# Optimization experiments

Measured on AMD Instinct MI355X. Metric: run time of the kernel, lower is better.

Reference implementation:

```python
import jax, jax.numpy as jnp
import numpy as np

N_NODES = 50000
N_EDGES = 1600000
NODE_DIM = 64
EDGE_DIM = 32
HIDDEN = 128
OUT = 64


def setup_inputs() -> dict:
    key = jax.random.key(0)
    k1, k2, k3, k4, k5, k6, k7 = jax.random.split(key, 7)
    edge_index = jax.random.randint(k1, (2, N_EDGES), 0, N_NODES, dtype=jnp.int64 if jax.config.jax_enable_x64 else jnp.int32)
    node_features = jax.random.normal(k2, (N_NODES, NODE_DIM), dtype=jnp.float32)
    edge_features = jax.random.normal(k3, (N_EDGES, EDGE_DIM), dtype=jnp.float32)
    in_dim = EDGE_DIM + 2 * NODE_DIM
    # torch nn.Linear init scale ~ 1/sqrt(fan_in)
    W1 = jax.random.uniform(k4, (HIDDEN, in_dim), jnp.float32, -1.0, 1.0) / np.sqrt(in_dim)
    b1 = jax.random.uniform(k5, (HIDDEN,), jnp.float32, -1.0, 1.0) / np.sqrt(in_dim)
    W2 = jax.random.uniform(k6, (OUT, HIDDEN), jnp.float32, -1.0, 1.0) / np.sqrt(HIDDEN)
    b2 = jax.random.uniform(k7, (OUT,), jnp.float32, -1.0, 1.0) / np.sqrt(HIDDEN)
    return {"edge_index": edge_index, "node_features": node_features,
            "edge_features": edge_features, "W1": W1, "b1": b1, "W2": W2, "b2": b2}


def reference(edge_index, node_features, edge_features, W1, b1, W2, b2):
    src = node_features[edge_index[0]]  # [E, node_dim]
    tgt = node_features[edge_index[1]]  # [E, node_dim]
    x = jnp.concatenate([edge_features, src, tgt], axis=1)  # [E, edge_dim + 2*node_dim]
    h = jax.nn.relu(x @ W1.T + b1)  # [E, hidden]
    return h @ W2.T + b2  # [E, out]
```

## Files before the change

### kernel.cpp

```cpp
#include <hip/hip_runtime.h>

typedef __bf16 bf16x4 __attribute__((ext_vector_type(4)));
typedef __bf16 bf16x8 __attribute__((ext_vector_type(8)));
typedef float  f32x4  __attribute__((ext_vector_type(4)));

#define XS 168
#define HS 136

__device__ inline f32x4 mfma16(bf16x8 a, bf16x8 b, f32x4 c) {
  return __builtin_amdgcn_mfma_f32_16x16x32_bf16(a, b, c, 0, 0, 0);
}

struct bf2 { __bf16 h, l; };
__device__ inline bf2 split(float x) {
  bf2 r;
  r.h = (__bf16)x;
  r.l = (__bf16)(x - (float)r.h);
  return r;
}

__global__ __launch_bounds__(256, 2) void edge_mlp(
    const int* __restrict__ eidx, const float* __restrict__ nf,
    const float* __restrict__ ef, const float* __restrict__ W1,
    const float* __restrict__ b1, const float* __restrict__ W2,
    const float* __restrict__ b2, float* __restrict__ out, int E)
{
  __shared__ __bf16 sXh[64 * XS];
  __shared__ __bf16 sXl[64 * XS];
  __shared__ __bf16 sHh[64 * HS];
  __shared__ __bf16 sHl[64 * HS];

  const int tid  = threadIdx.x;
  const int lane = tid & 63;
  const int wv   = tid >> 6;
  const int l16  = lane & 15;
  const int q    = lane >> 4;

  bf16x8 w1h[2][5], w1l[2][5];
#pragma unroll
  for (int nt = 0; nt < 2; ++nt) {
    const int j = 32 * wv + 16 * nt + l16;
#pragma unroll
    for (int kc = 0; kc < 5; ++kc) {
      const float* p = W1 + j * 160 + kc * 32 + q * 8;
#pragma unroll
      for (int i = 0; i < 8; ++i) {
        bf2 s = split(p[i]);
        w1h[nt][kc][i] = s.h;
        w1l[nt][kc][i] = s.l;
      }
    }
  }
  bf16x8 w2h[4], w2l[4];
  {
    const int o = 16 * wv + l16;
#pragma unroll
    for (int kc = 0; kc < 4; ++kc) {
      const float* p = W2 + o * 128 + kc * 32 + q * 8;
#pragma unroll
      for (int i = 0; i < 8; ++i) {
        bf2 s = split(p[i]);
        w2h[kc][i] = s.h;
        w2l[kc][i] = s.l;
      }
    }
  }
  const float b1j0 = b1[32 * wv + l16];
  const float b1j1 = b1[32 * wv + 16 + l16];
  const float b2o  = b2[16 * wv + l16];

  const float4* ef4 = (const float4*)ef;
  const float4* nf4 = (const float4*)nf;

  const int eL = tid >> 2;
  const int qq = tid & 3;
  const int ntiles = (E + 63) >> 6;

  for (int tile = blockIdx.x; tile < ntiles; tile += gridDim.x) {
    const int e0 = tile << 6;

    {
      int e = e0 + eL;
      if (e >= E) e = E - 1;
      const int s = eidx[e];
      const int t = eidx[E + e];
#pragma unroll
      for (int i = 0; i < 10; ++i) {
        const int fi = qq * 10 + i;
        const float4* p = (fi < 8)  ? (ef4 + e * 8 + fi)
                        : (fi < 24) ? (nf4 + s * 16 + (fi - 8))
                                    : (nf4 + t * 16 + (fi - 24));
        const float4 v = *p;
        bf16x4 hv, lv;
        { bf2 s0 = split(v.x); hv[0] = s0.h; lv[0] = s0.l; }
        { bf2 s1 = split(v.y); hv[1] = s1.h; lv[1] = s1.l; }
        { bf2 s2 = split(v.z); hv[2] = s2.h; lv[2] = s2.l; }
        { bf2 s3 = split(v.w); hv[3] = s3.h; lv[3] = s3.l; }
        *(bf16x4*)&sXh[eL * XS + fi * 4] = hv;
        *(bf16x4*)&sXl[eL * XS + fi * 4] = lv;
      }
    }
    __syncthreads();

    f32x4 acc1[4][2];
#pragma unroll
    for (int mt = 0; mt < 4; ++mt)
#pragma unroll
      for (int nt = 0; nt < 2; ++nt)
        acc1[mt][nt] = (f32x4){0.f, 0.f, 0.f, 0.f};

#pragma unroll
    for (int kc = 0; kc < 5; ++kc) {
#pragma unroll
      for (int mt = 0; mt < 4; ++mt) {
        const bf16x8 ah = *(const bf16x8*)&sXh[(16 * mt + l16) * XS + kc * 32 + q * 8];
        const bf16x8 al = *(const bf16x8*)&sXl[(16 * mt + l16) * XS + kc * 32 + q * 8];
#pragma unroll
        for (int nt = 0; nt < 2; ++nt) {
          acc1[mt][nt] = mfma16(ah, w1h[nt][kc], acc1[mt][nt]);
          acc1[mt][nt] = mfma16(ah, w1l[nt][kc], acc1[mt][nt]);
          acc1[mt][nt] = mfma16(al, w1h[nt][kc], acc1[mt][nt]);
        }
      }
    }

#pragma unroll
    for (int mt = 0; mt < 4; ++mt) {
#pragma unroll
      for (int nt = 0; nt < 2; ++nt) {
        const int col = 32 * wv + 16 * nt + l16;
        const float bb = nt ? b1j1 : b1j0;
#pragma unroll
        for (int r = 0; r < 4; ++r) {
          float h = acc1[mt][nt][r] + bb;
          h = fmaxf(h, 0.f);
          bf2 s = split(h);
          const int row = 16 * mt + 4 * q + r;
          sHh[row * HS + col] = s.h;
          sHl[row * HS + col] = s.l;
        }
      }
    }
    __syncthreads();

    f32x4 acc2[4];
#pragma unroll
    for (int mt = 0; mt < 4; ++mt) acc2[mt] = (f32x4){0.f, 0.f, 0.f, 0.f};
#pragma unroll
    for (int kc = 0; kc < 4; ++kc) {
#pragma unroll
      for (int mt = 0; mt < 4; ++mt) {
        const bf16x8 ah = *(const bf16x8*)&sHh[(16 * mt + l16) * HS + kc * 32 + q * 8];
        const bf16x8 al = *(const bf16x8*)&sHl[(16 * mt + l16) * HS + kc * 32 + q * 8];
        acc2[mt] = mfma16(ah, w2h[kc], acc2[mt]);
        acc2[mt] = mfma16(ah, w2l[kc], acc2[mt]);
        acc2[mt] = mfma16(al, w2h[kc], acc2[mt]);
      }
    }
#pragma unroll
    for (int mt = 0; mt < 4; ++mt) {
#pragma unroll
      for (int r = 0; r < 4; ++r) {
        const int e = e0 + 16 * mt + 4 * q + r;
        if (e < E) out[e * 64 + 16 * wv + l16] = acc2[mt][r] + b2o;
      }
    }
  }
}

extern "C" void kernel_launch(void* const* d_in, const int* in_sizes, int n_in,
                              void* d_out, int out_size, void* d_ws, size_t ws_size,
                              hipStream_t stream) {
  const int*   eidx = (const int*)d_in[0];
  const float* nf   = (const float*)d_in[1];
  const float* ef   = (const float*)d_in[2];
  const float* W1   = (const float*)d_in[3];
  const float* b1   = (const float*)d_in[4];
  const float* W2   = (const float*)d_in[5];
  const float* b2   = (const float*)d_in[6];
  float* out = (float*)d_out;
  const int E = in_sizes[0] / 2;

  dim3 grid(1024), block(256);
  hipLaunchKernelGGL(edge_mlp, grid, block, 0, stream,
                     eidx, nf, ef, W1, b1, W2, b2, out, E);
}
```

Measured before the change: 896.5 us.

## Prefetch next tile's gather into registers and interleave MFMA chains

Loads the next tile's edge and node features into registers while the current tile runs its MFMAs, overlapping global gather latency with compute. The gather layout now has each thread take strided float4s instead of contiguous ones, which improves coalescing. The MFMA issue order is changed so consecutive MFMAs use independent accumulators. The hidden split is packed into one u32 per element so stores are single 32-bit writes, and it is unpacked with perm instructions before the second GEMM. The cost is ten float4 prefetch registers per thread, which may pressure occupancy under the 2-wave-per-SIMD launch bound.

```diff
diff --git a/kernel.cpp b/kernel.cpp
--- a/kernel.cpp
+++ b/kernel.cpp
@@ -3,9 +3,10 @@
 typedef __bf16 bf16x4 __attribute__((ext_vector_type(4)));
 typedef __bf16 bf16x8 __attribute__((ext_vector_type(8)));
 typedef float  f32x4  __attribute__((ext_vector_type(4)));
-
-#define XS 168
-#define HS 136
+typedef unsigned int u32x4 __attribute__((ext_vector_type(4)));
+
+#define XS  168
+#define HS2 132
 
 __device__ inline f32x4 mfma16(bf16x8 a, bf16x8 b, f32x4 c) {
   return __builtin_amdgcn_mfma_f32_16x16x32_bf16(a, b, c, 0, 0, 0);
@@ -17,6 +18,9 @@
   r.h = (__bf16)x;
   r.l = (__bf16)(x - (float)r.h);
   return r;
+}
+__device__ inline unsigned int bfbits(__bf16 x) {
+  return (unsigned int)__builtin_bit_cast(unsigned short, x);
 }
 
 __global__ __launch_bounds__(256, 2) void edge_mlp(
@@ -27,8 +31,7 @@
 {
   __shared__ __bf16 sXh[64 * XS];
   __shared__ __bf16 sXl[64 * XS];
-  __shared__ __bf16 sHh[64 * HS];
-  __shared__ __bf16 sHl[64 * HS];
+  __shared__ unsigned int sH2[64 * HS2];
 
   const int tid  = threadIdx.x;
   const int lane = tid & 63;
@@ -76,31 +79,46 @@
   const int qq = tid & 3;
   const int ntiles = (E + 63) >> 6;
 
-  for (int tile = blockIdx.x; tile < ntiles; tile += gridDim.x) {
+  float4 g[10];
+  auto gather = [&](int tile_) {
+    int e = tile_ * 64 + eL;
+    if (e >= E) e = E - 1;
+    const int s = eidx[e];
+    const int t = eidx[E + e];
+#pragma unroll
+    for (int i = 0; i < 10; ++i) {
+      const int fi = qq + 4 * i;
+      const float4* p = (i < 2) ? (ef4 + e * 8 + fi)
+                      : (i < 6) ? (nf4 + s * 16 + (fi - 8))
+                                : (nf4 + t * 16 + (fi - 24));
+      g[i] = *p;
+    }
+  };
+
+  int tile = blockIdx.x;
+  if (tile < ntiles) gather(tile);
+
+  for (; tile < ntiles; tile += gridDim.x) {
     const int e0 = tile << 6;
 
+#pragma unroll
+    for (int i = 0; i < 10; ++i) {
+      const int fi = qq + 4 * i;
+      const float4 v = g[i];
+      bf16x4 hv, lv;
+      { bf2 s0 = split(v.x); hv[0] = s0.h; lv[0] = s0.l; }
+      { bf2 s1 = split(v.y); hv[1] = s1.h; lv[1] = s1.l; }
+      { bf2 s2 = split(v.z); hv[2] = s2.h; lv[2] = s2.l; }
+      { bf2 s3 = split(v.w); hv[3] = s3.h; lv[3] = s3.l; }
+      *(bf16x4*)&sXh[eL * XS + fi * 4] = hv;
+      *(bf16x4*)&sXl[eL * XS + fi * 4] = lv;
+    }
+    __syncthreads();
+
     {
-      int e = e0 + eL;
-      if (e >= E) e = E - 1;
-      const int s = eidx[e];
-      const int t = eidx[E + e];
-#pragma unroll
-      for (int i = 0; i < 10; ++i) {
-        const int fi = qq * 10 + i;
-        const float4* p = (fi < 8)  ? (ef4 + e * 8 + fi)
-                        : (fi < 24) ? (nf4 + s * 16 + (fi - 8))
-                                    : (nf4 + t * 16 + (fi - 24));
-        const float4 v = *p;
-        bf16x4 hv, lv;
-        { bf2 s0 = split(v.x); hv[0] = s0.h; lv[0] = s0.l; }
-        { bf2 s1 = split(v.y); hv[1] = s1.h; lv[1] = s1.l; }
-        { bf2 s2 = split(v.z); hv[2] = s2.h; lv[2] = s2.l; }
-        { bf2 s3 = split(v.w); hv[3] = s3.h; lv[3] = s3.l; }
-        *(bf16x4*)&sXh[eL * XS + fi * 4] = hv;
-        *(bf16x4*)&sXl[eL * XS + fi * 4] = lv;
-      }
-    }
-    __syncthreads();
+      const int nxt = tile + gridDim.x;
+      if (nxt < ntiles) gather(nxt);
+    }
 
     f32x4 acc1[4][2];
 #pragma unroll
@@ -112,15 +130,28 @@
 #pragma unroll
     for (int kc = 0; kc < 5; ++kc) {
 #pragma unroll
-      for (int mt = 0; mt < 4; ++mt) {
-        const bf16x8 ah = *(const bf16x8*)&sXh[(16 * mt + l16) * XS + kc * 32 + q * 8];
-        const bf16x8 al = *(const bf16x8*)&sXl[(16 * mt + l16) * XS + kc * 32 + q * 8];
-#pragma unroll
-        for (int nt = 0; nt < 2; ++nt) {
-          acc1[mt][nt] = mfma16(ah, w1h[nt][kc], acc1[mt][nt]);
-          acc1[mt][nt] = mfma16(ah, w1l[nt][kc], acc1[mt][nt]);
-          acc1[mt][nt] = mfma16(al, w1h[nt][kc], acc1[mt][nt]);
+      for (int mp = 0; mp < 4; mp += 2) {
+        bf16x8 ah[2], al[2];
+#pragma unroll
+        for (int m = 0; m < 2; ++m) {
+          ah[m] = *(const bf16x8*)&sXh[(16 * (mp + m) + l16) * XS + kc * 32 + q * 8];
+          al[m] = *(const bf16x8*)&sXl[(16 * (mp + m) + l16) * XS + kc * 32 + q * 8];
         }
+#pragma unroll
+        for (int m = 0; m < 2; ++m)
+#pragma unroll
+          for (int nt = 0; nt < 2; ++nt)
+            acc1[mp + m][nt] = mfma16(ah[m], w1h[nt][kc], acc1[mp + m][nt]);
+#pragma unroll
+        for (int m = 0; m < 2; ++m)
+#pragma unroll
+          for (int nt = 0; nt < 2; ++nt)
+            acc1[mp + m][nt] = mfma16(ah[m], w1l[nt][kc], acc1[mp + m][nt]);
+#pragma unroll
+        for (int m = 0; m < 2; ++m)
+#pragma unroll
+          for (int nt = 0; nt < 2; ++nt)
+            acc1[mp + m][nt] = mfma16(al[m], w1h[nt][kc], acc1[mp + m][nt]);
       }
     }
 
@@ -132,12 +163,9 @@
         const float bb = nt ? b1j1 : b1j0;
 #pragma unroll
         for (int r = 0; r < 4; ++r) {
-          float h = acc1[mt][nt][r] + bb;
-          h = fmaxf(h, 0.f);
+          float h = fmaxf(acc1[mt][nt][r] + bb, 0.f);
           bf2 s = split(h);
-          const int row = 16 * mt + 4 * q + r;
-          sHh[row * HS + col] = s.h;
-          sHl[row * HS + col] = s.l;
+          sH2[(16 * mt + 4 * q + r) * HS2 + col] = bfbits(s.h) | (bfbits(s.l) << 16);
         }
       }
     }
@@ -146,17 +174,35 @@
     f32x4 acc2[4];
 #pragma unroll
     for (int mt = 0; mt < 4; ++mt) acc2[mt] = (f32x4){0.f, 0.f, 0.f, 0.f};
+
 #pragma unroll
     for (int kc = 0; kc < 4; ++kc) {
+      bf16x8 ah[4], al[4];
 #pragma unroll
       for (int mt = 0; mt < 4; ++mt) {
-        const bf16x8 ah = *(const bf16x8*)&sHh[(16 * mt + l16) * HS + kc * 32 + q * 8];
-        const bf16x8 al = *(const bf16x8*)&sHl[(16 * mt + l16) * HS + kc * 32 + q * 8];
-        acc2[mt] = mfma16(ah, w2h[kc], acc2[mt]);
-        acc2[mt] = mfma16(ah, w2l[kc], acc2[mt]);
-        acc2[mt] = mfma16(al, w2h[kc], acc2[mt]);
-      }
-    }
+        const unsigned int* base = &sH2[(16 * mt + l16) * HS2 + kc * 32 + q * 8];
+        const u32x4 u0 = *(const u32x4*)base;
+        const u32x4 u1 = *(const u32x4*)(base + 4);
+        u32x4 hh, ll;
+        hh.x = __builtin_amdgcn_perm(u0.y, u0.x, 0x05040100u);
+        hh.y = __builtin_amdgcn_perm(u0.w, u0.z, 0x05040100u);
+        hh.z = __builtin_amdgcn_perm(u1.y, u1.x, 0x05040100u);
+        hh.w = __builtin_amdgcn_perm(u1.w, u1.z, 0x05040100u);
+        ll.x = __builtin_amdgcn_perm(u0.y, u0.x, 0x07060302u);
+        ll.y = __builtin_amdgcn_perm(u0.w, u0.z, 0x07060302u);
+        ll.z = __builtin_amdgcn_perm(u1.y, u1.x, 0x07060302u);
+        ll.w = __builtin_amdgcn_perm(u1.w, u1.z, 0x07060302u);
+        ah[mt] = __builtin_bit_cast(bf16x8, hh);
+        al[mt] = __builtin_bit_cast(bf16x8, ll);
+      }
+#pragma unroll
+      for (int mt = 0; mt < 4; ++mt) acc2[mt] = mfma16(ah[mt], w2h[kc], acc2[mt]);
+#pragma unroll
+      for (int mt = 0; mt < 4; ++mt) acc2[mt] = mfma16(ah[mt], w2l[kc], acc2[mt]);
+#pragma unroll
+      for (int mt = 0; mt < 4; ++mt) acc2[mt] = mfma16(al[mt], w2h[kc], acc2[mt]);
+    }
+
 #pragma unroll
     for (int mt = 0; mt < 4; ++mt) {
 #pragma unroll
```

Result: faster. 728.1 us (-18.8%).
